# Optimization experiments

Measured on AMD Instinct MI355X. Metric: run time of the kernel, lower is better.

## Reference

```python
import jax, jax.numpy as jnp
import numpy as np

N = 100000      # nodes
E = 3200000     # edges (avg degree 32)
IN, HID, OUT = 512, 256, 64
K = 10
ALPHA = 0.1


def setup_inputs() -> dict:
    key = jax.random.key(0)
    k1, k2, k3, k4 = jax.random.split(key, 4)
    x = jax.random.normal(k1, (N, IN), dtype=jnp.float32)
    edge_index = jax.random.randint(k2, (2, E), 0, N, dtype=jnp.int64)
    # MLP params (Kaiming-ish scaling)
    W1 = jax.random.normal(k3, (IN, HID), dtype=jnp.float32) / np.sqrt(IN)
    b1 = jnp.zeros((HID,), dtype=jnp.float32)
    W2 = jax.random.normal(k4, (HID, OUT), dtype=jnp.float32) / np.sqrt(HID)
    b2 = jnp.zeros((OUT,), dtype=jnp.float32)
    # GPR_prop PPR init: temp[k] = alpha*(1-alpha)^k, temp[K] = (1-alpha)^K
    ks = np.arange(K + 1)
    temp = ALPHA * (1.0 - ALPHA) ** ks
    temp[-1] = (1.0 - ALPHA) ** K
    temp = jnp.asarray(temp, dtype=jnp.float32)
    return {"x": x, "edge_index": edge_index, "W1": W1, "b1": b1,
            "W2": W2, "b2": b2, "temp": temp}


def reference(x, edge_index, W1, b1, W2, b2, temp):
    # MLP front-end (eval mode: dropout = identity)
    h = jax.nn.relu(x @ W1 + b1)
    h = h @ W2 + b2                                  # [N, OUT]

    # gcn_norm with self-loops: A_hat = D^{-1/2} (A + I) D^{-1/2}
    loop = jnp.arange(N, dtype=edge_index.dtype)
    src = jnp.concatenate([edge_index[0], loop])      # [E+N]
    dst = jnp.concatenate([edge_index[1], loop])      # [E+N]
    deg = jax.ops.segment_sum(jnp.ones_like(dst, dtype=h.dtype), dst,
                              num_segments=N)
    dis = jnp.where(deg > 0, jax.lax.rsqrt(deg), 0.0)
    norm = (dis[src] * dis[dst])[:, None]             # [E+N, 1]

    # GPR propagation: out = sum_k temp[k] * A_hat^k h
    def step(carry, gamma):
        hk, acc = carry
        hk = jax.ops.segment_sum(norm * hk[src], dst, num_segments=N)
        return (hk, acc + gamma * hk), None

    (_, out), _ = jax.lax.scan(step, (h, temp[0] * h), temp[1:])
    return out
```

## Files before the change

kernel.cpp:

```cpp
#include <hip/hip_runtime.h>

#define NN 100000
#define NE 3200000
#define DIN 512
#define DHID 256
#define DOUT 64
#define KPROP 10

typedef _Float16 f16;
typedef _Float16 f16x8 __attribute__((ext_vector_type(8)));
typedef _Float16 f16x4 __attribute__((ext_vector_type(4)));
typedef float f32x4 __attribute__((ext_vector_type(4)));

__global__ void detect_i64(const int* __restrict__ ei, int* __restrict__ flag) {
  int lane = threadIdx.x;
  int ok = 1;
  for (int i = lane; i < 512; i += 64)
    if (ei[2 * i + 1] != 0) ok = 0;
  ok = __all(ok);
  if (lane == 0) *flag = ok;
}

__global__ void zero_cnt(int* __restrict__ cnt) {
  int g = blockIdx.x * blockDim.x + threadIdx.x;
  if (g < NN) cnt[g] = 0;
}

__global__ void count_deg(const int* __restrict__ ei, const int* __restrict__ flag,
                          int* __restrict__ cnt, int* __restrict__ rank) {
  int g = blockIdx.x * blockDim.x + threadIdx.x;
  int e0 = g * 4;
  if (e0 >= NE) return;
  int is64 = *flag;
  int d0, d1, d2, d3;
  if (is64) {
    int4 a = *(const int4*)&ei[2 * (size_t)NE + 2 * (size_t)e0];
    int4 b = *(const int4*)&ei[2 * (size_t)NE + 2 * (size_t)e0 + 4];
    d0 = a.x; d1 = a.z; d2 = b.x; d3 = b.z;
  } else {
    int4 a = *(const int4*)&ei[(size_t)NE + e0];
    d0 = a.x; d1 = a.y; d2 = a.z; d3 = a.w;
  }
  int4 rk;
  rk.x = atomicAdd(&cnt[d0], 1);
  rk.y = atomicAdd(&cnt[d1], 1);
  rk.z = atomicAdd(&cnt[d2], 1);
  rk.w = atomicAdd(&cnt[d3], 1);
  *(int4*)&rank[e0] = rk;
}

__global__ void scan1(const int* __restrict__ cnt, int* __restrict__ rs,
                      int* __restrict__ bsum) {
  __shared__ int tmp[1024];
  int t = threadIdx.x;
  int g = blockIdx.x * 1024 + t;
  int v = (g < NN) ? cnt[g] : 0;
  tmp[t] = v;
  __syncthreads();
  for (int off = 1; off < 1024; off <<= 1) {
    int y = (t >= off) ? tmp[t - off] : 0;
    __syncthreads();
    tmp[t] += y;
    __syncthreads();
  }
  if (g < NN) rs[g] = tmp[t] - v;
  if (t == 1023) bsum[blockIdx.x] = tmp[t];
}

__global__ void scan2(int* __restrict__ bsum, int nb) {
  if (blockIdx.x == 0 && threadIdx.x == 0) {
    int s = 0;
    for (int i = 0; i < nb; i++) { int v = bsum[i]; bsum[i] = s; s += v; }
  }
}

__global__ void scan3_and_dis(int* __restrict__ rs, const int* __restrict__ bsum,
                              const int* __restrict__ cnt, float* __restrict__ dis) {
  int g = blockIdx.x * blockDim.x + threadIdx.x;
  if (g < NN) {
    rs[g] = rs[g] + bsum[g >> 10];
    dis[g] = rsqrtf((float)(cnt[g] + 1));
  }
}

__global__ void fill_csr(const int* __restrict__ ei, const int* __restrict__ flag,
                         const float* __restrict__ dis, const int* __restrict__ rs,
                         const int* __restrict__ rank, int2* __restrict__ recs) {
  int g = blockIdx.x * blockDim.x + threadIdx.x;
  int e0 = g * 4;
  if (e0 >= NE) return;
  int is64 = *flag;
  int s[4], d[4];
  if (is64) {
    int4 a = *(const int4*)&ei[2 * (size_t)NE + 2 * (size_t)e0];
    int4 b = *(const int4*)&ei[2 * (size_t)NE + 2 * (size_t)e0 + 4];
    d[0] = a.x; d[1] = a.z; d[2] = b.x; d[3] = b.z;
    int4 c = *(const int4*)&ei[2 * (size_t)e0];
    int4 e = *(const int4*)&ei[2 * (size_t)e0 + 4];
    s[0] = c.x; s[1] = c.z; s[2] = e.x; s[3] = e.z;
  } else {
    int4 a = *(const int4*)&ei[(size_t)NE + e0];
    d[0] = a.x; d[1] = a.y; d[2] = a.z; d[3] = a.w;
    int4 c = *(const int4*)&ei[e0];
    s[0] = c.x; s[1] = c.y; s[2] = c.z; s[3] = c.w;
  }
  int4 rk = *(const int4*)&rank[e0];
  int rka[4] = { rk.x, rk.y, rk.z, rk.w };
  #pragma unroll
  for (int j = 0; j < 4; j++) {
    int pos = rs[d[j]] + rka[j];
    recs[pos] = make_int2(s[j], __float_as_int(dis[s[j]] * dis[d[j]]));
  }
}

__global__ void cvt_weights(const float* __restrict__ W1, const float* __restrict__ W2,
                            f16* __restrict__ W1t, f16* __restrict__ W2t) {
  int g = blockIdx.x * 256 + threadIdx.x;
  if (g < DIN * DHID) {
    int k = g >> 8, n = g & 255;
    W1t[(size_t)n * DIN + k] = (f16)W1[g];
  }
  if (g < DHID * DOUT) {
    int k = g >> 6, n = g & 63;
    W2t[(size_t)n * DHID + k] = (f16)W2[g];
  }
}

__global__ __launch_bounds__(256) void mlp_mfma(
    const float* __restrict__ x, const f16* __restrict__ W1t,
    const float* __restrict__ b1, const f16* __restrict__ W2t,
    const float* __restrict__ b2, const float* __restrict__ temp,
    f16* __restrict__ h, f16* __restrict__ z)
{
  __shared__ __align__(16) char smraw[2 * 64 * 136 * 2];
  f16* xsb = (f16*)smraw;
  f16* h1s = (f16*)smraw;
  int t = threadIdx.x;
  int lane = t & 63;
  int w = t >> 6;
  int n0 = blockIdx.x * 64;
  int r15 = lane & 15;
  int g4 = lane >> 4;
  int nbase = w * 64;
  int srow = t >> 5, sc4 = t & 31;

  f32x4 acc[4][4];
  #pragma unroll
  for (int nt = 0; nt < 4; nt++) {
    float bv = b1[nbase + nt * 16 + r15];
    #pragma unroll
    for (int mt = 0; mt < 4; mt++) acc[mt][nt] = (f32x4){bv, bv, bv, bv};
  }

  float4 ld[8];
  #pragma unroll
  for (int it = 0; it < 8; it++) {
    int row = srow + it * 8;
    int gr = n0 + row;
    ld[it] = (gr < NN) ? *(const float4*)&x[(size_t)gr * DIN + sc4 * 4]
                       : make_float4(0.f, 0.f, 0.f, 0.f);
  }
  #pragma unroll
  for (int it = 0; it < 8; it++) {
    int row = srow + it * 8;
    f16x4 hv = { (f16)ld[it].x, (f16)ld[it].y, (f16)ld[it].z, (f16)ld[it].w };
    *(f16x4*)&xsb[row * 136 + sc4 * 4] = hv;
  }
  __syncthreads();

  for (int c = 0; c < 4; c++) {
    int cur = c & 1;
    if (c < 3) {
      #pragma unroll
      for (int it = 0; it < 8; it++) {
        int row = srow + it * 8;
        int gr = n0 + row;
        ld[it] = (gr < NN)
            ? *(const float4*)&x[(size_t)gr * DIN + (c + 1) * 128 + sc4 * 4]
            : make_float4(0.f, 0.f, 0.f, 0.f);
      }
    }
    int k0 = c * 128;
    const f16* xs = xsb + cur * 8704;
    #pragma unroll
    for (int ks = 0; ks < 4; ks++) {
      int kk = ks * 32 + g4 * 8;
      f16x8 a[4], b[4];
      #pragma unroll
      for (int mt = 0; mt < 4; mt++)
        a[mt] = *(const f16x8*)&xs[(mt * 16 + r15) * 136 + kk];
      #pragma unroll
      for (int nt = 0; nt < 4; nt++)
        b[nt] = *(const f16x8*)&W1t[(size_t)(nbase + nt * 16 + r15) * DIN + k0 + kk];
      #pragma unroll
      for (int mt = 0; mt < 4; mt++)
        #pragma unroll
        for (int nt = 0; nt < 4; nt++)
          acc[mt][nt] = __builtin_amdgcn_mfma_f32_16x16x32_f16(a[mt], b[nt], acc[mt][nt], 0, 0, 0);
    }
    if (c < 3) {
      #pragma unroll
      for (int it = 0; it < 8; it++) {
        int row = srow + it * 8;
        f16x4 hv = { (f16)ld[it].x, (f16)ld[it].y, (f16)ld[it].z, (f16)ld[it].w };
        *(f16x4*)&xsb[(cur ^ 1) * 8704 + row * 136 + sc4 * 4] = hv;
      }
    }
    __syncthreads();
  }

  #pragma unroll
  for (int mt = 0; mt < 4; mt++)
    #pragma unroll
    for (int nt = 0; nt < 4; nt++)
      #pragma unroll
      for (int r = 0; r < 4; r++) {
        float v = fmaxf(acc[mt][nt][r], 0.f);
        h1s[(mt * 16 + g4 * 4 + r) * 264 + nbase + nt * 16 + r15] = (f16)v;
      }
  __syncthreads();

  f32x4 acc2[4];
  #pragma unroll
  for (int nt = 0; nt < 4; nt++) {
    float bv = b2[nt * 16 + r15];
    acc2[nt] = (f32x4){bv, bv, bv, bv};
  }
  #pragma unroll
  for (int ks = 0; ks < 8; ks++) {
    int kk = ks * 32 + g4 * 8;
    f16x8 a2 = *(const f16x8*)&h1s[(w * 16 + r15) * 264 + kk];
    #pragma unroll
    for (int nt = 0; nt < 4; nt++) {
      f16x8 bf = *(const f16x8*)&W2t[(size_t)(nt * 16 + r15) * DHID + kk];
      acc2[nt] = __builtin_amdgcn_mfma_f32_16x16x32_f16(a2, bf, acc2[nt], 0, 0, 0);
    }
  }
  float tK = temp[KPROP];
  #pragma unroll
  for (int nt = 0; nt < 4; nt++)
    #pragma unroll
    for (int r = 0; r < 4; r++) {
      int node = n0 + w * 16 + g4 * 4 + r;
      if (node < NN) {
        int colv = nt * 16 + r15;
        float v = acc2[nt][r];
        h[(size_t)node * DOUT + colv] = (f16)v;
        z[(size_t)node * DOUT + colv] = (f16)(tK * v);
      }
    }
}

__global__ __launch_bounds__(256) void prop_horner(
    const f16* __restrict__ z, f16* __restrict__ zn, const f16* __restrict__ h,
    float* __restrict__ out, const int* __restrict__ rs, const int* __restrict__ cnt,
    const int2* __restrict__ recs, const float* __restrict__ dis,
    const float* __restrict__ temp, int kidx, int final_step)
{
  int w = blockIdx.x * 4 + (threadIdx.x >> 6);
  int lane = threadIdx.x & 63;
  if (w >= NN) return;
  int q = lane >> 3;
  int s8 = lane & 7;

  float acc[8];
  #pragma unroll
  for (int f = 0; f < 8; f++) acc[f] = 0.f;

  int beg = rs[w], n = cnt[w];
  const int2* rp = recs + beg;

  int e = 0;
  for (; e + 32 <= n; e += 32) {
    int2 r0 = rp[e + q];
    int2 r1 = rp[e + 8 + q];
    int2 r2 = rp[e + 16 + q];
    int2 r3 = rp[e + 24 + q];
    f16x8 g0 = *(const f16x8*)&z[(size_t)r0.x * DOUT + s8 * 8];
    f16x8 g1 = *(const f16x8*)&z[(size_t)r1.x * DOUT + s8 * 8];
    f16x8 g2 = *(const f16x8*)&z[(size_t)r2.x * DOUT + s8 * 8];
    f16x8 g3 = *(const f16x8*)&z[(size_t)r3.x * DOUT + s8 * 8];
    float w0 = __int_as_float(r0.y);
    float w1 = __int_as_float(r1.y);
    float w2 = __int_as_float(r2.y);
    float w3 = __int_as_float(r3.y);
    #pragma unroll
    for (int f = 0; f < 8; f++) acc[f] = fmaf(w0, (float)g0[f], acc[f]);
    #pragma unroll
    for (int f = 0; f < 8; f++) acc[f] = fmaf(w1, (float)g1[f], acc[f]);
    #pragma unroll
    for (int f = 0; f < 8; f++) acc[f] = fmaf(w2, (float)g2[f], acc[f]);
    #pragma unroll
    for (int f = 0; f < 8; f++) acc[f] = fmaf(w3, (float)g3[f], acc[f]);
  }
  for (; e + 8 <= n; e += 8) {
    int2 r0 = rp[e + q];
    f16x8 g0 = *(const f16x8*)&z[(size_t)r0.x * DOUT + s8 * 8];
    float w0 = __int_as_float(r0.y);
    #pragma unroll
    for (int f = 0; f < 8; f++) acc[f] = fmaf(w0, (float)g0[f], acc[f]);
  }
  if (e < n) {
    int rem = n - e;
    int qq = q < rem ? q : rem - 1;
    int2 r0 = rp[e + qq];
    f16x8 g0 = *(const f16x8*)&z[(size_t)r0.x * DOUT + s8 * 8];
    float w0 = (q < rem) ? __int_as_float(r0.y) : 0.f;
    #pragma unroll
    for (int f = 0; f < 8; f++) acc[f] = fmaf(w0, (float)g0[f], acc[f]);
  }

  #pragma unroll
  for (int f = 0; f < 8; f++) {
    acc[f] += __shfl_xor(acc[f], 8);
    acc[f] += __shfl_xor(acc[f], 16);
    acc[f] += __shfl_xor(acc[f], 32);
  }

  if (q == 0) {
    float dd = dis[w];
    float dd2 = dd * dd;
    float gk = temp[kidx];
    f16x8 zs = *(const f16x8*)&z[(size_t)w * DOUT + s8 * 8];
    f16x8 hs = *(const f16x8*)&h[(size_t)w * DOUT + s8 * 8];
    #pragma unroll
    for (int f = 0; f < 8; f++)
      acc[f] += dd2 * (float)zs[f] + gk * (float)hs[f];
    if (final_step) {
      float4 o0 = { acc[0], acc[1], acc[2], acc[3] };
      float4 o1 = { acc[4], acc[5], acc[6], acc[7] };
      *(float4*)&out[(size_t)w * DOUT + s8 * 8] = o0;
      *(float4*)&out[(size_t)w * DOUT + s8 * 8 + 4] = o1;
    } else {
      f16x8 o;
      #pragma unroll
      for (int f = 0; f < 8; f++) o[f] = (f16)acc[f];
      *(f16x8*)&zn[(size_t)w * DOUT + s8 * 8] = o;
    }
  }
}

extern "C" void kernel_launch(void* const* d_in, const int* in_sizes, int n_in,
                              void* d_out, int out_size, void* d_ws, size_t ws_size,
                              hipStream_t stream) {
  const float* x    = (const float*)d_in[0];
  const int*   ei   = (const int*)d_in[1];
  const float* W1   = (const float*)d_in[2];
  const float* b1   = (const float*)d_in[3];
  const float* W2   = (const float*)d_in[4];
  const float* b2   = (const float*)d_in[5];
  const float* temp = (const float*)d_in[6];
  float* out = (float*)d_out;

  char* wsb = (char*)d_ws;
  size_t off = 0;
  auto carve = [&](size_t bytes) -> void* {
    void* p = wsb + off;
    off = (off + bytes + 255) & ~(size_t)255;
    return p;
  };
  int*   cnt    = (int*)carve((size_t)NN * 4);
  int*   rs     = (int*)carve((size_t)NN * 4);
  int*   bsum   = (int*)carve(128 * 4);
  int*   flag   = (int*)carve(256);
  float* dis    = (float*)carve((size_t)NN * 4);
  int*   rank   = (int*)carve((size_t)NE * 4);
  int2*  recs   = (int2*)carve((size_t)NE * 8);
  f16*   W1t    = (f16*)carve((size_t)DHID * DIN * 2);
  f16*   W2t    = (f16*)carve((size_t)DOUT * DHID * 2);
  f16*   h_buf  = (f16*)carve((size_t)NN * DOUT * 2);
  f16*   z_a    = (f16*)carve((size_t)NN * DOUT * 2);
  f16*   z_b    = (f16*)carve((size_t)NN * DOUT * 2);
  if (off > ws_size) return;

  detect_i64<<<1, 64, 0, stream>>>(ei, flag);
  zero_cnt<<<(NN + 255) / 256, 256, 0, stream>>>(cnt);
  count_deg<<<(NE / 4 + 255) / 256, 256, 0, stream>>>(ei, flag, cnt, rank);
  scan1<<<(NN + 1023) / 1024, 1024, 0, stream>>>(cnt, rs, bsum);
  scan2<<<1, 64, 0, stream>>>(bsum, (NN + 1023) / 1024);
  scan3_and_dis<<<(NN + 255) / 256, 256, 0, stream>>>(rs, bsum, cnt, dis);
  fill_csr<<<(NE / 4 + 255) / 256, 256, 0, stream>>>(ei, flag, dis, rs, rank, recs);

  cvt_weights<<<(DIN * DHID + 255) / 256, 256, 0, stream>>>(W1, W2, W1t, W2t);
  mlp_mfma<<<(NN + 63) / 64, 256, 0, stream>>>(x, W1t, b1, W2t, b2, temp, h_buf, z_a);

  const f16* zc = z_a;
  f16* zn = z_b;
  for (int k = KPROP - 1; k >= 0; k--) {
    prop_horner<<<(NN + 3) / 4, 256, 0, stream>>>(zc, zn, h_buf, out, rs, cnt,
                                                  recs, dis, temp, k, k == 0);
    const f16* t2 = zn;
    zn = (f16*)zc;
    zc = t2;
  }
}
```

Baseline: 972.2 us.

## Build CSR with tiled LDS histograms instead of global atomics

```diff
diff --git a/kernel.cpp b/kernel.cpp
--- a/kernel.cpp
+++ b/kernel.cpp
@@ -6,6 +6,11 @@
 #define DHID 256
 #define DOUT 64
 #define KPROP 10
+#define TSH 13
+#define TMSK 8191
+#define NT 13
+#define NCH 32
+#define CHSZ (NE / NCH)
 
 typedef _Float16 f16;
 typedef _Float16 f16x8 __attribute__((ext_vector_type(8)));
@@ -21,40 +26,49 @@
   if (lane == 0) *flag = ok;
 }
 
-__global__ void zero_cnt(int* __restrict__ cnt) {
-  int g = blockIdx.x * blockDim.x + threadIdx.x;
-  if (g < NN) cnt[g] = 0;
-}
-
-__global__ void count_deg(const int* __restrict__ ei, const int* __restrict__ flag,
-                          int* __restrict__ cnt, int* __restrict__ rank) {
-  int g = blockIdx.x * blockDim.x + threadIdx.x;
-  int e0 = g * 4;
-  if (e0 >= NE) return;
+__global__ __launch_bounds__(256) void count_tile(
+    const int* __restrict__ ei, const int* __restrict__ flag,
+    int* __restrict__ pc ) {
+  int t = blockIdx.x >> 5;
+  int c = blockIdx.x & 31;
+  __shared__ int lc[8192];
+  for (int j = threadIdx.x; j < 8192; j += 256) lc[j] = 0;
+  __syncthreads();
   int is64 = *flag;
-  int d0, d1, d2, d3;
-  if (is64) {
-    int4 a = *(const int4*)&ei[2 * (size_t)NE + 2 * (size_t)e0];
-    int4 b = *(const int4*)&ei[2 * (size_t)NE + 2 * (size_t)e0 + 4];
-    d0 = a.x; d1 = a.z; d2 = b.x; d3 = b.z;
-  } else {
-    int4 a = *(const int4*)&ei[(size_t)NE + e0];
-    d0 = a.x; d1 = a.y; d2 = a.z; d3 = a.w;
-  }
-  int4 rk;
-  rk.x = atomicAdd(&cnt[d0], 1);
-  rk.y = atomicAdd(&cnt[d1], 1);
-  rk.z = atomicAdd(&cnt[d2], 1);
-  rk.w = atomicAdd(&cnt[d3], 1);
-  *(int4*)&rank[e0] = rk;
-}
-
-__global__ void scan1(const int* __restrict__ cnt, int* __restrict__ rs,
+  const int* dstp = ei + (is64 ? 2 * (size_t)NE : (size_t)NE);
+  int st = is64 ? 2 : 1;
+  int end = (c + 1) * CHSZ;
+  for (int i = c * CHSZ + threadIdx.x; i < end; i += 256) {
+    int d = dstp[(size_t)i * st];
+    if ((d >> TSH) == t) atomicAdd(&lc[d & TMSK], 1);
+  }
+  __syncthreads();
+  for (int j = threadIdx.x; j < 8192; j += 256)
+    pc[((size_t)t * NCH + c) * 8192 + j] = lc[j];
+}
+
+__global__ void tile_offsets(int* __restrict__ pc, int* __restrict__ deg) {
+  int g = blockIdx.x * 256 + threadIdx.x;
+  if (g >= NT * 8192) return;
+  int t = g >> TSH, j = g & TMSK;
+  int run = 0;
+  #pragma unroll 4
+  for (int c = 0; c < NCH; c++) {
+    size_t idx = ((size_t)t * NCH + c) * 8192 + j;
+    int v = pc[idx];
+    pc[idx] = run;
+    run += v;
+  }
+  int node = (t << TSH) + j;
+  if (node < NN) deg[node] = run;
+}
+
+__global__ void scan1(const int* __restrict__ deg, int* __restrict__ rs,
                       int* __restrict__ bsum) {
   __shared__ int tmp[1024];
   int t = threadIdx.x;
   int g = blockIdx.x * 1024 + t;
-  int v = (g < NN) ? cnt[g] : 0;
+  int v = (g < NN) ? deg[g] : 0;
   tmp[t] = v;
   __syncthreads();
   for (int off = 1; off < 1024; off <<= 1) {
@@ -75,41 +89,39 @@
 }
 
 __global__ void scan3_and_dis(int* __restrict__ rs, const int* __restrict__ bsum,
-                              const int* __restrict__ cnt, float* __restrict__ dis) {
+                              const int* __restrict__ deg, float* __restrict__ dis) {
   int g = blockIdx.x * blockDim.x + threadIdx.x;
   if (g < NN) {
     rs[g] = rs[g] + bsum[g >> 10];
-    dis[g] = rsqrtf((float)(cnt[g] + 1));
-  }
-}
-
-__global__ void fill_csr(const int* __restrict__ ei, const int* __restrict__ flag,
-                         const float* __restrict__ dis, const int* __restrict__ rs,
-                         const int* __restrict__ rank, int2* __restrict__ recs) {
-  int g = blockIdx.x * blockDim.x + threadIdx.x;
-  int e0 = g * 4;
-  if (e0 >= NE) return;
+    dis[g] = rsqrtf((float)(deg[g] + 1));
+  }
+}
+
+__global__ __launch_bounds__(256) void fill_tile(
+    const int* __restrict__ ei, const int* __restrict__ flag,
+    const float* __restrict__ dis, const int* __restrict__ rs,
+    const int* __restrict__ pc, int2* __restrict__ recs) {
+  int t = blockIdx.x >> 5;
+  int c = blockIdx.x & 31;
+  __shared__ int cur[8192];
+  int tb = t << TSH;
+  for (int j = threadIdx.x; j < 8192; j += 256) {
+    int node = tb + j;
+    cur[j] = (node < NN) ? rs[node] + pc[((size_t)t * NCH + c) * 8192 + j] : 0;
+  }
+  __syncthreads();
   int is64 = *flag;
-  int s[4], d[4];
-  if (is64) {
-    int4 a = *(const int4*)&ei[2 * (size_t)NE + 2 * (size_t)e0];
-    int4 b = *(const int4*)&ei[2 * (size_t)NE + 2 * (size_t)e0 + 4];
-    d[0] = a.x; d[1] = a.z; d[2] = b.x; d[3] = b.z;
-    int4 c = *(const int4*)&ei[2 * (size_t)e0];
-    int4 e = *(const int4*)&ei[2 * (size_t)e0 + 4];
-    s[0] = c.x; s[1] = c.z; s[2] = e.x; s[3] = e.z;
-  } else {
-    int4 a = *(const int4*)&ei[(size_t)NE + e0];
-    d[0] = a.x; d[1] = a.y; d[2] = a.z; d[3] = a.w;
-    int4 c = *(const int4*)&ei[e0];
-    s[0] = c.x; s[1] = c.y; s[2] = c.z; s[3] = c.w;
-  }
-  int4 rk = *(const int4*)&rank[e0];
-  int rka[4] = { rk.x, rk.y, rk.z, rk.w };
-  #pragma unroll
-  for (int j = 0; j < 4; j++) {
-    int pos = rs[d[j]] + rka[j];
-    recs[pos] = make_int2(s[j], __float_as_int(dis[s[j]] * dis[d[j]]));
+  const int* srcp = ei;
+  const int* dstp = ei + (is64 ? 2 * (size_t)NE : (size_t)NE);
+  int st = is64 ? 2 : 1;
+  int end = (c + 1) * CHSZ;
+  for (int i = c * CHSZ + threadIdx.x; i < end; i += 256) {
+    int d = dstp[(size_t)i * st];
+    if ((d >> TSH) == t) {
+      int s = srcp[(size_t)i * st];
+      int p = atomicAdd(&cur[d & TMSK], 1);
+      recs[p] = make_int2(s, __float_as_int(dis[s] * dis[d]));
+    }
   }
 }
 
@@ -253,7 +265,7 @@
 
 __global__ __launch_bounds__(256) void prop_horner(
     const f16* __restrict__ z, f16* __restrict__ zn, const f16* __restrict__ h,
-    float* __restrict__ out, const int* __restrict__ rs, const int* __restrict__ cnt,
+    float* __restrict__ out, const int* __restrict__ rs, const int* __restrict__ rs1,
     const int2* __restrict__ recs, const float* __restrict__ dis,
     const float* __restrict__ temp, int kidx, int final_step)
 {
@@ -267,7 +279,8 @@
   #pragma unroll
   for (int f = 0; f < 8; f++) acc[f] = 0.f;
 
-  int beg = rs[w], n = cnt[w];
+  int beg = rs[w];
+  int n = ((w < NN - 1) ? rs1[w] : NE) - beg;
   const int2* rp = recs + beg;
 
   int e = 0;
@@ -359,12 +372,12 @@
     off = (off + bytes + 255) & ~(size_t)255;
     return p;
   };
-  int*   cnt    = (int*)carve((size_t)NN * 4);
+  int*   pc     = (int*)carve((size_t)NT * NCH * 8192 * 4);
+  int*   deg    = (int*)carve((size_t)NN * 4);
   int*   rs     = (int*)carve((size_t)NN * 4);
   int*   bsum   = (int*)carve(128 * 4);
   int*   flag   = (int*)carve(256);
   float* dis    = (float*)carve((size_t)NN * 4);
-  int*   rank   = (int*)carve((size_t)NE * 4);
   int2*  recs   = (int2*)carve((size_t)NE * 8);
   f16*   W1t    = (f16*)carve((size_t)DHID * DIN * 2);
   f16*   W2t    = (f16*)carve((size_t)DOUT * DHID * 2);
@@ -374,12 +387,12 @@
   if (off > ws_size) return;
 
   detect_i64<<<1, 64, 0, stream>>>(ei, flag);
-  zero_cnt<<<(NN + 255) / 256, 256, 0, stream>>>(cnt);
-  count_deg<<<(NE / 4 + 255) / 256, 256, 0, stream>>>(ei, flag, cnt, rank);
-  scan1<<<(NN + 1023) / 1024, 1024, 0, stream>>>(cnt, rs, bsum);
+  count_tile<<<NT * NCH, 256, 0, stream>>>(ei, flag, pc);
+  tile_offsets<<<(NT * 8192 + 255) / 256, 256, 0, stream>>>(pc, deg);
+  scan1<<<(NN + 1023) / 1024, 1024, 0, stream>>>(deg, rs, bsum);
   scan2<<<1, 64, 0, stream>>>(bsum, (NN + 1023) / 1024);
-  scan3_and_dis<<<(NN + 255) / 256, 256, 0, stream>>>(rs, bsum, cnt, dis);
-  fill_csr<<<(NE / 4 + 255) / 256, 256, 0, stream>>>(ei, flag, dis, rs, rank, recs);
+  scan3_and_dis<<<(NN + 255) / 256, 256, 0, stream>>>(rs, bsum, deg, dis);
+  fill_tile<<<NT * NCH, 256, 0, stream>>>(ei, flag, dis, rs, pc, recs);
 
   cvt_weights<<<(DIN * DHID + 255) / 256, 256, 0, stream>>>(W1, W2, W1t, W2t);
   mlp_mfma<<<(NN + 63) / 64, 256, 0, stream>>>(x, W1t, b1, W2t, b2, temp, h_buf, z_a);
@@ -387,7 +400,7 @@
   const f16* zc = z_a;
   f16* zn = z_b;
   for (int k = KPROP - 1; k >= 0; k--) {
-    prop_horner<<<(NN + 3) / 4, 256, 0, stream>>>(zc, zn, h_buf, out, rs, cnt,
+    prop_horner<<<(NN + 3) / 4, 256, 0, stream>>>(zc, zn, h_buf, out, rs, rs + 1,
                                                   recs, dis, temp, k, k == 0);
     const f16* t2 = zn;
     zn = (f16*)zc;
```

Measured after the change: 1.213 ms. +24.8%, slower.

## Factor symmetric normalization into pre-scaled features and drop per-edge weights

Applied to the files above, without the earlier changes.

```diff
diff --git a/kernel.cpp b/kernel.cpp
--- a/kernel.cpp
+++ b/kernel.cpp
@@ -84,8 +84,8 @@
 }
 
 __global__ void fill_csr(const int* __restrict__ ei, const int* __restrict__ flag,
-                         const float* __restrict__ dis, const int* __restrict__ rs,
-                         const int* __restrict__ rank, int2* __restrict__ recs) {
+                         const int* __restrict__ rs, const int* __restrict__ rank,
+                         int* __restrict__ col) {
   int g = blockIdx.x * blockDim.x + threadIdx.x;
   int e0 = g * 4;
   if (e0 >= NE) return;
@@ -107,10 +107,8 @@
   int4 rk = *(const int4*)&rank[e0];
   int rka[4] = { rk.x, rk.y, rk.z, rk.w };
   #pragma unroll
-  for (int j = 0; j < 4; j++) {
-    int pos = rs[d[j]] + rka[j];
-    recs[pos] = make_int2(s[j], __float_as_int(dis[s[j]] * dis[d[j]]));
-  }
+  for (int j = 0; j < 4; j++)
+    col[rs[d[j]] + rka[j]] = s[j];
 }
 
 __global__ void cvt_weights(const float* __restrict__ W1, const float* __restrict__ W2,
@@ -130,7 +128,7 @@
     const float* __restrict__ x, const f16* __restrict__ W1t,
     const float* __restrict__ b1, const f16* __restrict__ W2t,
     const float* __restrict__ b2, const float* __restrict__ temp,
-    f16* __restrict__ h, f16* __restrict__ z)
+    const float* __restrict__ dis, f16* __restrict__ h, f16* __restrict__ zs)
 {
   __shared__ __align__(16) char smraw[2 * 64 * 136 * 2];
   f16* xsb = (f16*)smraw;
@@ -238,23 +236,25 @@
   }
   float tK = temp[KPROP];
   #pragma unroll
-  for (int nt = 0; nt < 4; nt++)
-    #pragma unroll
-    for (int r = 0; r < 4; r++) {
-      int node = n0 + w * 16 + g4 * 4 + r;
-      if (node < NN) {
+  for (int r = 0; r < 4; r++) {
+    int node = n0 + w * 16 + g4 * 4 + r;
+    if (node < NN) {
+      float dv = dis[node] * tK;
+      #pragma unroll
+      for (int nt = 0; nt < 4; nt++) {
         int colv = nt * 16 + r15;
         float v = acc2[nt][r];
         h[(size_t)node * DOUT + colv] = (f16)v;
-        z[(size_t)node * DOUT + colv] = (f16)(tK * v);
+        zs[(size_t)node * DOUT + colv] = (f16)(dv * v);
       }
     }
+  }
 }
 
 __global__ __launch_bounds__(256) void prop_horner(
-    const f16* __restrict__ z, f16* __restrict__ zn, const f16* __restrict__ h,
+    const f16* __restrict__ zs, f16* __restrict__ zsn, const f16* __restrict__ h,
     float* __restrict__ out, const int* __restrict__ rs, const int* __restrict__ cnt,
-    const int2* __restrict__ recs, const float* __restrict__ dis,
+    const int* __restrict__ col, const float* __restrict__ dis,
     const float* __restrict__ temp, int kidx, int final_step)
 {
   int w = blockIdx.x * 4 + (threadIdx.x >> 6);
@@ -263,51 +263,51 @@
   int q = lane >> 3;
   int s8 = lane & 7;
 
+  float dd = dis[w];
+  float gk = temp[kidx];
+  f16x8 zself = *(const f16x8*)&zs[(size_t)w * DOUT + s8 * 8];
+  f16x8 hs = *(const f16x8*)&h[(size_t)w * DOUT + s8 * 8];
+
   float acc[8];
   #pragma unroll
   for (int f = 0; f < 8; f++) acc[f] = 0.f;
 
   int beg = rs[w], n = cnt[w];
-  const int2* rp = recs + beg;
+  const int* cp = col + beg;
 
   int e = 0;
   for (; e + 32 <= n; e += 32) {
-    int2 r0 = rp[e + q];
-    int2 r1 = rp[e + 8 + q];
-    int2 r2 = rp[e + 16 + q];
-    int2 r3 = rp[e + 24 + q];
-    f16x8 g0 = *(const f16x8*)&z[(size_t)r0.x * DOUT + s8 * 8];
-    f16x8 g1 = *(const f16x8*)&z[(size_t)r1.x * DOUT + s8 * 8];
-    f16x8 g2 = *(const f16x8*)&z[(size_t)r2.x * DOUT + s8 * 8];
-    f16x8 g3 = *(const f16x8*)&z[(size_t)r3.x * DOUT + s8 * 8];
-    float w0 = __int_as_float(r0.y);
-    float w1 = __int_as_float(r1.y);
-    float w2 = __int_as_float(r2.y);
-    float w3 = __int_as_float(r3.y);
-    #pragma unroll
-    for (int f = 0; f < 8; f++) acc[f] = fmaf(w0, (float)g0[f], acc[f]);
-    #pragma unroll
-    for (int f = 0; f < 8; f++) acc[f] = fmaf(w1, (float)g1[f], acc[f]);
-    #pragma unroll
-    for (int f = 0; f < 8; f++) acc[f] = fmaf(w2, (float)g2[f], acc[f]);
-    #pragma unroll
-    for (int f = 0; f < 8; f++) acc[f] = fmaf(w3, (float)g3[f], acc[f]);
+    int c0 = cp[e + q];
+    int c1 = cp[e + 8 + q];
+    int c2 = cp[e + 16 + q];
+    int c3 = cp[e + 24 + q];
+    f16x8 g0 = *(const f16x8*)&zs[(size_t)c0 * DOUT + s8 * 8];
+    f16x8 g1 = *(const f16x8*)&zs[(size_t)c1 * DOUT + s8 * 8];
+    f16x8 g2 = *(const f16x8*)&zs[(size_t)c2 * DOUT + s8 * 8];
+    f16x8 g3 = *(const f16x8*)&zs[(size_t)c3 * DOUT + s8 * 8];
+    #pragma unroll
+    for (int f = 0; f < 8; f++) acc[f] += (float)g0[f];
+    #pragma unroll
+    for (int f = 0; f < 8; f++) acc[f] += (float)g1[f];
+    #pragma unroll
+    for (int f = 0; f < 8; f++) acc[f] += (float)g2[f];
+    #pragma unroll
+    for (int f = 0; f < 8; f++) acc[f] += (float)g3[f];
   }
   for (; e + 8 <= n; e += 8) {
-    int2 r0 = rp[e + q];
-    f16x8 g0 = *(const f16x8*)&z[(size_t)r0.x * DOUT + s8 * 8];
-    float w0 = __int_as_float(r0.y);
-    #pragma unroll
-    for (int f = 0; f < 8; f++) acc[f] = fmaf(w0, (float)g0[f], acc[f]);
+    int c0 = cp[e + q];
+    f16x8 g0 = *(const f16x8*)&zs[(size_t)c0 * DOUT + s8 * 8];
+    #pragma unroll
+    for (int f = 0; f < 8; f++) acc[f] += (float)g0[f];
   }
   if (e < n) {
     int rem = n - e;
     int qq = q < rem ? q : rem - 1;
-    int2 r0 = rp[e + qq];
-    f16x8 g0 = *(const f16x8*)&z[(size_t)r0.x * DOUT + s8 * 8];
-    float w0 = (q < rem) ? __int_as_float(r0.y) : 0.f;
-    #pragma unroll
-    for (int f = 0; f < 8; f++) acc[f] = fmaf(w0, (float)g0[f], acc[f]);
+    int c0 = cp[e + qq];
+    f16x8 g0 = *(const f16x8*)&zs[(size_t)c0 * DOUT + s8 * 8];
+    float m = (q < rem) ? 1.f : 0.f;
+    #pragma unroll
+    for (int f = 0; f < 8; f++) acc[f] = fmaf(m, (float)g0[f], acc[f]);
   }
 
   #pragma unroll
@@ -318,24 +318,20 @@
   }
 
   if (q == 0) {
-    float dd = dis[w];
-    float dd2 = dd * dd;
-    float gk = temp[kidx];
-    f16x8 zs = *(const f16x8*)&z[(size_t)w * DOUT + s8 * 8];
-    f16x8 hs = *(const f16x8*)&h[(size_t)w * DOUT + s8 * 8];
+    float zv[8];
     #pragma unroll
     for (int f = 0; f < 8; f++)
-      acc[f] += dd2 * (float)zs[f] + gk * (float)hs[f];
+      zv[f] = gk * (float)hs[f] + dd * (acc[f] + (float)zself[f]);
     if (final_step) {
-      float4 o0 = { acc[0], acc[1], acc[2], acc[3] };
-      float4 o1 = { acc[4], acc[5], acc[6], acc[7] };
+      float4 o0 = { zv[0], zv[1], zv[2], zv[3] };
+      float4 o1 = { zv[4], zv[5], zv[6], zv[7] };
       *(float4*)&out[(size_t)w * DOUT + s8 * 8] = o0;
       *(float4*)&out[(size_t)w * DOUT + s8 * 8 + 4] = o1;
     } else {
       f16x8 o;
       #pragma unroll
-      for (int f = 0; f < 8; f++) o[f] = (f16)acc[f];
-      *(f16x8*)&zn[(size_t)w * DOUT + s8 * 8] = o;
+      for (int f = 0; f < 8; f++) o[f] = (f16)(dd * zv[f]);
+      *(f16x8*)&zsn[(size_t)w * DOUT + s8 * 8] = o;
     }
   }
 }
@@ -365,12 +361,12 @@
   int*   flag   = (int*)carve(256);
   float* dis    = (float*)carve((size_t)NN * 4);
   int*   rank   = (int*)carve((size_t)NE * 4);
-  int2*  recs   = (int2*)carve((size_t)NE * 8);
+  int*   colA   = (int*)carve((size_t)NE * 4);
   f16*   W1t    = (f16*)carve((size_t)DHID * DIN * 2);
   f16*   W2t    = (f16*)carve((size_t)DOUT * DHID * 2);
   f16*   h_buf  = (f16*)carve((size_t)NN * DOUT * 2);
-  f16*   z_a    = (f16*)carve((size_t)NN * DOUT * 2);
-  f16*   z_b    = (f16*)carve((size_t)NN * DOUT * 2);
+  f16*   zs_a   = (f16*)carve((size_t)NN * DOUT * 2);
+  f16*   zs_b   = (f16*)carve((size_t)NN * DOUT * 2);
   if (off > ws_size) return;
 
   detect_i64<<<1, 64, 0, stream>>>(ei, flag);
@@ -379,16 +375,17 @@
   scan1<<<(NN + 1023) / 1024, 1024, 0, stream>>>(cnt, rs, bsum);
   scan2<<<1, 64, 0, stream>>>(bsum, (NN + 1023) / 1024);
   scan3_and_dis<<<(NN + 255) / 256, 256, 0, stream>>>(rs, bsum, cnt, dis);
-  fill_csr<<<(NE / 4 + 255) / 256, 256, 0, stream>>>(ei, flag, dis, rs, rank, recs);
+  fill_csr<<<(NE / 4 + 255) / 256, 256, 0, stream>>>(ei, flag, rs, rank, colA);
 
   cvt_weights<<<(DIN * DHID + 255) / 256, 256, 0, stream>>>(W1, W2, W1t, W2t);
-  mlp_mfma<<<(NN + 63) / 64, 256, 0, stream>>>(x, W1t, b1, W2t, b2, temp, h_buf, z_a);
-
-  const f16* zc = z_a;
-  f16* zn = z_b;
+  mlp_mfma<<<(NN + 63) / 64, 256, 0, stream>>>(x, W1t, b1, W2t, b2, temp, dis,
+                                               h_buf, zs_a);
+
+  const f16* zc = zs_a;
+  f16* zn = zs_b;
   for (int k = KPROP - 1; k >= 0; k--) {
     prop_horner<<<(NN + 3) / 4, 256, 0, stream>>>(zc, zn, h_buf, out, rs, cnt,
-                                                  recs, dis, temp, k, k == 0);
+                                                  colA, dis, temp, k, k == 0);
     const f16* t2 = zn;
     zn = (f16*)zc;
     zc = t2;
```

Measured after the change: 906.8 us. 6.7% less time.
